# Kernel optimization log

Measured on AMD Instinct MI355X. Metric: run time of the kernel, lower is better.

The kernel has to match this reference:

```python
import jax, jax.numpy as jnp
import numpy as np

N_NODES = 100000
N_EDGES = 1600000
HIDDEN = 64


def setup_inputs() -> dict:
    key = jax.random.key(0)
    ks = jax.random.split(key, 12)
    x = jax.random.normal(ks[0], (N_NODES, HIDDEN), dtype=jnp.float32)
    edge_index = jax.random.randint(ks[1], (2, N_EDGES), 0, N_NODES, dtype=jnp.int64)
    s = 1.0 / np.sqrt(HIDDEN)  # glorot-ish scale for 64x64 linears
    params = {}
    for li, base in enumerate([2, 5, 8]):
        i = li + 1
        params[f"W_l{i}"] = jax.random.uniform(ks[base], (HIDDEN, HIDDEN), jnp.float32, -s, s)
        params[f"b_l{i}"] = jnp.zeros((HIDDEN,), jnp.float32)
        params[f"W_r{i}"] = jax.random.uniform(ks[base + 1], (HIDDEN, HIDDEN), jnp.float32, -s, s)
    return {"x": x, "edge_index": edge_index, **params}


def _sage_conv(x, src, dst, W_l, b_l, W_r):
    # mean-aggregate source features onto targets (PyG SAGEConv, aggr='mean')
    agg = jax.ops.segment_sum(x[src], dst, num_segments=N_NODES)  # [N, d]
    deg = jax.ops.segment_sum(jnp.ones_like(dst, dtype=x.dtype), dst, num_segments=N_NODES)
    agg = agg / jnp.maximum(deg, 1.0)[:, None]
    # out = lin_l(agg) + lin_r(x)
    return agg @ W_l + b_l + x @ W_r


def reference(x, edge_index, W_l1, b_l1, W_r1, W_l2, b_l2, W_r2, W_l3, b_l3, W_r3):
    src, dst = edge_index[0], edge_index[1]
    # eval mode: dropout is identity
    h = jax.nn.elu(_sage_conv(x, src, dst, W_l1, b_l1, W_r1))
    h = jax.nn.elu(_sage_conv(h, src, dst, W_l2, b_l2, W_r2))
    h = jax.nn.elu(_sage_conv(h, src, dst, W_l3, b_l3, W_r3))
    return h
```

## Files before the change

kernel.cpp:

```cpp
#include <hip/hip_runtime.h>
#include <hip/hip_bf16.h>
#include <math.h>


#define HID   64
#define SB    512
#define MAXSB 256
#define SCAP  10240
#define CHUNK 8192

__device__ __forceinline__ float b2f(unsigned short u) {
    unsigned int t = ((unsigned int)u) << 16;
    return __uint_as_float(t);
}
__device__ __forceinline__ unsigned short f2b(float f) {
    unsigned int u = __float_as_uint(f);
    u = (u + 0x7FFF + ((u >> 16) & 1)) >> 16;
    return (unsigned short)u;
}


__launch_bounds__(256)
__global__ void partition_edges(const int* __restrict__ src, const int* __restrict__ dst,
                                unsigned int* __restrict__ part, int* __restrict__ gcnt,
                                int E) {
    __shared__ unsigned int stage[CHUNK];
    __shared__ int lcnt[MAXSB];
    __shared__ int lbase[MAXSB];
    __shared__ int lrun[MAXSB];
    __shared__ int gpos[MAXSB];
    __shared__ int tmp[MAXSB];
    int tid = threadIdx.x;
    int e0 = blockIdx.x * CHUNK, e1 = min(e0 + CHUNK, E);

    lcnt[tid] = 0;
    __syncthreads();
    for (int e = e0 + tid; e < e1; e += 256)
        atomicAdd(&lcnt[dst[e] >> 9], 1);
    __syncthreads();
    int v = lcnt[tid];
    tmp[tid] = v;
    __syncthreads();
    for (int off = 1; off < 256; off <<= 1) {
        int u = (tid >= off) ? tmp[tid - off] : 0;
        __syncthreads();
        tmp[tid] += u;
        __syncthreads();
    }
    lbase[tid] = tmp[tid] - v;
    lrun[tid]  = tmp[tid] - v;
    __syncthreads();
    for (int e = e0 + tid; e < e1; e += 256) {
        int d = dst[e];
        int s = d >> 9;
        int pos = atomicAdd(&lrun[s], 1);
        stage[pos] = ((unsigned)(d & 511) << 17) | (unsigned)src[e];
    }
    __syncthreads();
    {
        int c = lcnt[tid];
        gpos[tid] = c ? atomicAdd(&gcnt[tid], c) : 0;
    }
    __syncthreads();
    for (int s = 0; s < MAXSB; ++s) {
        int c = lcnt[s];
        if (c == 0) continue;
        int gp = gpos[s];
        int c2 = min(c, max(SCAP - gp, 0));
        unsigned int* dp = part + (size_t)s * SCAP + gp;
        const unsigned int* sp = &stage[lbase[s]];
        for (int j = tid; j < c2; j += 256) dp[j] = sp[j];
    }
}


__launch_bounds__(256)
__global__ void sub_count(const unsigned int* __restrict__ part,
                          const int* __restrict__ gcnt, int* __restrict__ cnt, int N) {
    __shared__ int lcnt[SB];
    int s = blockIdx.x;
    int sz = min(gcnt[s], SCAP);
    const unsigned int* slab = part + (size_t)s * SCAP;
    for (int i = threadIdx.x; i < SB; i += 256) lcnt[i] = 0;
    __syncthreads();
    for (int i = threadIdx.x; i < sz; i += 256)
        atomicAdd(&lcnt[slab[i] >> 17], 1);
    __syncthreads();
    int base = s * SB;
    for (int i = threadIdx.x; i < SB; i += 256)
        if (base + i < N) cnt[base + i] = lcnt[i];
}


__launch_bounds__(256)
__global__ void sub_fill(const unsigned int* __restrict__ part,
                         const int* __restrict__ gcnt, const int* __restrict__ offs,
                         int* __restrict__ csr, int N) {
    __shared__ unsigned int stage[SCAP];
    __shared__ int lrun[SB];
    int s = blockIdx.x;
    int sz = min(gcnt[s], SCAP);
    const unsigned int* slab = part + (size_t)s * SCAP;
    int base = s * SB;
    int gbase = offs[base];
    for (int i = threadIdx.x; i < SB; i += 256) {
        int node = base + i;
        lrun[i] = offs[min(node, N)] - gbase;
    }
    __syncthreads();
    for (int i = threadIdx.x; i < sz; i += 256) {
        unsigned int u = slab[i];
        int pos = atomicAdd(&lrun[u >> 17], 1);
        stage[pos] = u & 0x1FFFF;
    }
    __syncthreads();
    int total = offs[min(base + SB, N)] - gbase;
    for (int j = threadIdx.x; j < total; j += 256)
        csr[gbase + j] = (int)stage[j];
}


__global__ void scan_partials(const int* __restrict__ cnt, int* __restrict__ bsum, int n) {
    __shared__ int lsum[256];
    int t = threadIdx.x;
    int base = blockIdx.x * 1024 + t * 4;
    int s = 0;
    if (base + 3 < n) {
        int4 v = *(const int4*)&cnt[base];
        s = v.x + v.y + v.z + v.w;
    } else {
        for (int i = 0; i < 4; ++i) if (base + i < n) s += cnt[base + i];
    }
    lsum[t] = s;
    __syncthreads();
    for (int off = 128; off > 0; off >>= 1) {
        if (t < off) lsum[t] += lsum[t + off];
        __syncthreads();
    }
    if (t == 0) bsum[blockIdx.x] = lsum[0];
}

__global__ void scan_tops(int* __restrict__ bsum, int* __restrict__ offs_last,
                          int nb, int E) {
    __shared__ int s[128];
    int t = threadIdx.x;
    s[t] = (t < nb) ? bsum[t] : 0;
    __syncthreads();
    for (int off = 1; off < 128; off <<= 1) {
        int v = (t >= off) ? s[t - off] : 0;
        __syncthreads();
        s[t] += v;
        __syncthreads();
    }
    if (t < nb) bsum[t] = (t == 0) ? 0 : s[t - 1];
    if (t == 0) *offs_last = E;
}

__global__ void scan_write(const int* __restrict__ cnt, const int* __restrict__ bsum,
                           int* __restrict__ offs, int n) {
    __shared__ int lsum[256];
    int t = threadIdx.x;
    int base = blockIdx.x * 1024 + t * 4;
    int v0 = 0, v1 = 0, v2 = 0, v3 = 0;
    bool full = (base + 3 < n);
    if (full) {
        int4 v = *(const int4*)&cnt[base];
        v0 = v.x; v1 = v.y; v2 = v.z; v3 = v.w;
    } else {
        if (base     < n) v0 = cnt[base];
        if (base + 1 < n) v1 = cnt[base + 1];
        if (base + 2 < n) v2 = cnt[base + 2];
        if (base + 3 < n) v3 = cnt[base + 3];
    }
    lsum[t] = v0 + v1 + v2 + v3;
    __syncthreads();
    for (int off = 1; off < 256; off <<= 1) {
        int u = (t >= off) ? lsum[t - off] : 0;
        __syncthreads();
        lsum[t] += u;
        __syncthreads();
    }
    int ex = bsum[blockIdx.x] + ((t == 0) ? 0 : lsum[t - 1]);
    int o0 = ex, o1 = ex + v0, o2 = o1 + v1, o3 = o2 + v2;
    if (full) {
        *(int4*)&offs[base] = make_int4(o0, o1, o2, o3);
    } else {
        if (base     < n) offs[base]     = o0;
        if (base + 1 < n) offs[base + 1] = o1;
        if (base + 2 < n) offs[base + 2] = o2;
        if (base + 3 < n) offs[base + 3] = o3;
    }
}


__global__ void to_bf16(const float* __restrict__ in, unsigned short* __restrict__ o, int n4) {
    int i = blockIdx.x * blockDim.x + threadIdx.x;
    if (i < n4) {
        float4 v = ((const float4*)in)[i];
        ushort4 u;
        u.x = f2b(v.x); u.y = f2b(v.y); u.z = f2b(v.z); u.w = f2b(v.w);
        ((ushort4*)o)[i] = u;
    }
}


__launch_bounds__(256)
__global__ void gather_mean(const unsigned short* __restrict__ hb,
                            const int* __restrict__ offs, const int* __restrict__ csr,
                            unsigned short* __restrict__ agg, int nnodes) {
    int lane = threadIdx.x & 63;
    int wv   = threadIdx.x >> 6;
    int wid  = blockIdx.x * 4 + wv;
    int nw   = gridDim.x * 4;
    for (int n = wid; n < nnodes; n += nw) {
        int beg = offs[n], end = offs[n + 1];
        int deg = end - beg;
        float a0 = 0.f, a1 = 0.f, a2 = 0.f, a3 = 0.f;
        float a4 = 0.f, a5 = 0.f, a6 = 0.f, a7 = 0.f;
        for (int base = beg; base < end; base += 64) {
            int cnt = min(64, end - base);
            int myi = csr[base + min(lane, cnt - 1)];
            int j = 0;
            for (; j + 8 <= cnt; j += 8) {
                int s0 = __shfl(myi, j + 0), s1 = __shfl(myi, j + 1);
                int s2 = __shfl(myi, j + 2), s3 = __shfl(myi, j + 3);
                int s4 = __shfl(myi, j + 4), s5 = __shfl(myi, j + 5);
                int s6 = __shfl(myi, j + 6), s7 = __shfl(myi, j + 7);
                a0 += b2f(hb[(size_t)s0 * HID + lane]);
                a1 += b2f(hb[(size_t)s1 * HID + lane]);
                a2 += b2f(hb[(size_t)s2 * HID + lane]);
                a3 += b2f(hb[(size_t)s3 * HID + lane]);
                a4 += b2f(hb[(size_t)s4 * HID + lane]);
                a5 += b2f(hb[(size_t)s5 * HID + lane]);
                a6 += b2f(hb[(size_t)s6 * HID + lane]);
                a7 += b2f(hb[(size_t)s7 * HID + lane]);
            }
            for (; j < cnt; ++j) {
                int s = __shfl(myi, j);
                a0 += b2f(hb[(size_t)s * HID + lane]);
            }
        }
        float m = (((a0 + a1) + (a2 + a3)) + ((a4 + a5) + (a6 + a7)))
                  * (1.0f / (float)max(deg, 1));
        agg[(size_t)n * HID + lane] = f2b(m);
    }
}


__launch_bounds__(256)
__global__ void dense_cat(const unsigned short* __restrict__ aggb,
                          const unsigned short* __restrict__ hb,
                          const float* __restrict__ Wl, const float* __restrict__ bl,
                          const float* __restrict__ Wr,
                          float* __restrict__ outf, unsigned short* __restrict__ out_bf,
                          int nrows) {
    __shared__ float W_s[128][64];
    __shared__ float cat_s[32][132];
    __shared__ float bl_s[64];
    int tid = threadIdx.x;
    int n0  = blockIdx.x * 32;

    for (int idx = tid; idx < 2048; idx += 256) {
        int f = idx >> 4, c4 = (idx & 15) * 4;
        const float* Wsrc = (f < 64) ? (Wl + f * 64 + c4) : (Wr + (f - 64) * 64 + c4);
        *(float4*)&W_s[f][c4] = *(const float4*)Wsrc;
    }
    if (tid < 64) bl_s[tid] = bl[tid];

    for (int idx = tid; idx < 1024; idx += 256) {
        int r = idx >> 5, c4 = idx & 31;
        float4 v = make_float4(0.f, 0.f, 0.f, 0.f);
        if (n0 + r < nrows) {
            const unsigned short* sp = (c4 < 16)
                ? (aggb + (size_t)(n0 + r) * HID + c4 * 4)
                : (hb   + (size_t)(n0 + r) * HID + (c4 - 16) * 4);
            ushort4 u = *(const ushort4*)sp;
            v = make_float4(b2f(u.x), b2f(u.y), b2f(u.z), b2f(u.w));
        }
        *(float4*)&cat_s[r][c4 * 4] = v;
    }
    __syncthreads();

    int cg = tid & 15, rg = tid >> 4;
    int c0 = cg * 4, r0 = rg * 2;
    float acc0x = 0.f, acc0y = 0.f, acc0z = 0.f, acc0w = 0.f;
    float acc1x = 0.f, acc1y = 0.f, acc1z = 0.f, acc1w = 0.f;

    for (int k = 0; k < 128; k += 4) {
        float4 a0 = *(float4*)&cat_s[r0 + 0][k];
        float4 a1 = *(float4*)&cat_s[r0 + 1][k];
#pragma unroll
        for (int u = 0; u < 4; ++u) {
            float4 w = *(float4*)&W_s[k + u][c0];
            float av0 = (&a0.x)[u], av1 = (&a1.x)[u];
            acc0x += av0 * w.x; acc0y += av0 * w.y;
            acc0z += av0 * w.z; acc0w += av0 * w.w;
            acc1x += av1 * w.x; acc1y += av1 * w.y;
            acc1z += av1 * w.z; acc1w += av1 * w.w;
        }
    }

    float bx = bl_s[c0], by = bl_s[c0 + 1], bz = bl_s[c0 + 2], bw = bl_s[c0 + 3];
#pragma unroll
    for (int i = 0; i < 2; ++i) {
        int row = n0 + r0 + i;
        if (row < nrows) {
            float4 o;
            o.x = (i ? acc1x : acc0x) + bx;
            o.y = (i ? acc1y : acc0y) + by;
            o.z = (i ? acc1z : acc0z) + bz;
            o.w = (i ? acc1w : acc0w) + bw;
            o.x = o.x > 0.f ? o.x : expm1f(o.x);
            o.y = o.y > 0.f ? o.y : expm1f(o.y);
            o.z = o.z > 0.f ? o.z : expm1f(o.z);
            o.w = o.w > 0.f ? o.w : expm1f(o.w);
            if (outf) *(float4*)&outf[(size_t)row * HID + c0] = o;
            if (out_bf) {
                ushort4 u;
                u.x = f2b(o.x); u.y = f2b(o.y); u.z = f2b(o.z); u.w = f2b(o.w);
                *(ushort4*)&out_bf[(size_t)row * HID + c0] = u;
            }
        }
    }
}


extern "C" void kernel_launch(void* const* d_in, const int* in_sizes, int n_in,
                              void* d_out, int out_size, void* d_ws, size_t ws_size,
                              hipStream_t stream) {
    const float* x   = (const float*)d_in[0];
    const int*   ei  = (const int*)d_in[1];
    const float* Wl1 = (const float*)d_in[2];
    const float* bl1 = (const float*)d_in[3];
    const float* Wr1 = (const float*)d_in[4];
    const float* Wl2 = (const float*)d_in[5];
    const float* bl2 = (const float*)d_in[6];
    const float* Wr2 = (const float*)d_in[7];
    const float* Wl3 = (const float*)d_in[8];
    const float* bl3 = (const float*)d_in[9];
    const float* Wr3 = (const float*)d_in[10];
    float* out = (float*)d_out;

    int N = in_sizes[0] / HID;
    int E = in_sizes[1] / 2;
    const int* src = ei;
    const int* dst = ei + E;

    int nsb = (N + SB - 1) / SB;
    int PB  = (E + CHUNK - 1) / CHUNK;
    int sb  = (N + 1023) / 1024;

    char* p = (char*)d_ws;
    unsigned short* aggB = (unsigned short*)p; p += (size_t)N * HID * 2;
    unsigned short* bfX  = (unsigned short*)p; p += (size_t)N * HID * 2;
    unsigned short* bf1  = (unsigned short*)p; p += (size_t)N * HID * 2;
    unsigned short* bf2  = (unsigned short*)p; p += (size_t)N * HID * 2;
    int*            csr  = (int*)p;            p += (size_t)E * sizeof(int);
    int*            cnt  = (int*)p;            p += (size_t)N * sizeof(int);
    int*            offs = (int*)p;            p += (size_t)(N + 4) * sizeof(int);
    int*            bsum = (int*)p;            p += 256 * sizeof(int);
    int*            gcnt = (int*)p;            p += MAXSB * sizeof(int);
    unsigned int*   part = (unsigned int*)p;   p += (size_t)MAXSB * SCAP * 4;

    hipMemsetAsync(gcnt, 0, MAXSB * sizeof(int), stream);

    partition_edges<<<PB, 256, 0, stream>>>(src, dst, part, gcnt, E);
    sub_count<<<nsb, 256, 0, stream>>>(part, gcnt, cnt, N);
    scan_partials<<<sb, 256, 0, stream>>>(cnt, bsum, N);
    scan_tops<<<1, 128, 0, stream>>>(bsum, &offs[N], sb, E);
    scan_write<<<sb, 256, 0, stream>>>(cnt, bsum, offs, N);
    sub_fill<<<nsb, 256, 0, stream>>>(part, gcnt, offs, csr, N);

    to_bf16<<<(N * HID / 4 + 255) / 256, 256, 0, stream>>>(x, bfX, N * HID / 4);

    int db = (N + 31) / 32;

    gather_mean<<<2048, 256, 0, stream>>>(bfX, offs, csr, aggB, N);
    dense_cat<<<db, 256, 0, stream>>>(aggB, bfX, Wl1, bl1, Wr1, (float*)nullptr, bf1, N);

    gather_mean<<<2048, 256, 0, stream>>>(bf1, offs, csr, aggB, N);
    dense_cat<<<db, 256, 0, stream>>>(aggB, bf1, Wl2, bl2, Wr2, (float*)nullptr, bf2, N);

    gather_mean<<<2048, 256, 0, stream>>>(bf2, offs, csr, aggB, N);
    dense_cat<<<db, 256, 0, stream>>>(aggB, bf2, Wl3, bl3, Wr3, out, (unsigned short*)nullptr, N);
}
```

Baseline: 445.0 us.

## Shrink partition chunks, use wave-shuffle scan, flatten per-bucket scatter loop

Cuts the edges per partition block from 8192 to 2048, so the grid has four times as many blocks. The shared-memory Hillis-Steele scan, which needed many block barriers, becomes a wavefront shuffle scan plus a small cross-wave offset. The serial loop over 256 buckets in the write-out becomes one flat loop over staged edges, using a per-edge bucket byte to find each global position. This removes barrier and serialization overhead, at the cost of more global atomics on the bucket counters and less contiguous write-out.

After: 404.0 us. 9.2% less time.

```diff
diff --git a/kernel.cpp b/kernel.cpp
--- a/kernel.cpp
+++ b/kernel.cpp
@@ -7,7 +7,7 @@
 #define SB    512
 #define MAXSB 256
 #define SCAP  10240
-#define CHUNK 8192
+#define CHUNK 2048
 
 __device__ __forceinline__ float b2f(unsigned short u) {
     unsigned int t = ((unsigned int)u) << 16;
@@ -25,36 +25,45 @@
                                 unsigned int* __restrict__ part, int* __restrict__ gcnt,
                                 int E) {
     __shared__ unsigned int stage[CHUNK];
+    __shared__ unsigned char sbkt[CHUNK];
     __shared__ int lcnt[MAXSB];
     __shared__ int lbase[MAXSB];
     __shared__ int lrun[MAXSB];
     __shared__ int gpos[MAXSB];
-    __shared__ int tmp[MAXSB];
-    int tid = threadIdx.x;
+    __shared__ int wtot[4];
+    int tid = threadIdx.x, w = tid >> 6, lane = tid & 63;
     int e0 = blockIdx.x * CHUNK, e1 = min(e0 + CHUNK, E);
+    int ne = e1 - e0;
+    if (ne <= 0) return;
 
     lcnt[tid] = 0;
     __syncthreads();
     for (int e = e0 + tid; e < e1; e += 256)
         atomicAdd(&lcnt[dst[e] >> 9], 1);
     __syncthreads();
-    int v = lcnt[tid];
-    tmp[tid] = v;
-    __syncthreads();
-    for (int off = 1; off < 256; off <<= 1) {
-        int u = (tid >= off) ? tmp[tid - off] : 0;
-        __syncthreads();
-        tmp[tid] += u;
-        __syncthreads();
-    }
-    lbase[tid] = tmp[tid] - v;
-    lrun[tid]  = tmp[tid] - v;
+    {
+        int orig = lcnt[tid];
+        int v = orig;
+#pragma unroll
+        for (int off = 1; off < 64; off <<= 1) {
+            int u = __shfl_up(v, off);
+            if (lane >= off) v += u;
+        }
+        if (lane == 63) wtot[w] = v;
+        __syncthreads();
+        int woff = 0;
+        for (int i = 0; i < w; ++i) woff += wtot[i];
+        int excl = v + woff - orig;
+        lbase[tid] = excl;
+        lrun[tid]  = excl;
+    }
     __syncthreads();
     for (int e = e0 + tid; e < e1; e += 256) {
         int d = dst[e];
         int s = d >> 9;
         int pos = atomicAdd(&lrun[s], 1);
         stage[pos] = ((unsigned)(d & 511) << 17) | (unsigned)src[e];
+        sbkt[pos]  = (unsigned char)s;
     }
     __syncthreads();
     {
@@ -62,14 +71,10 @@
         gpos[tid] = c ? atomicAdd(&gcnt[tid], c) : 0;
     }
     __syncthreads();
-    for (int s = 0; s < MAXSB; ++s) {
-        int c = lcnt[s];
-        if (c == 0) continue;
-        int gp = gpos[s];
-        int c2 = min(c, max(SCAP - gp, 0));
-        unsigned int* dp = part + (size_t)s * SCAP + gp;
-        const unsigned int* sp = &stage[lbase[s]];
-        for (int j = tid; j < c2; j += 256) dp[j] = sp[j];
+    for (int j = tid; j < ne; j += 256) {
+        int s = sbkt[j];
+        int gp = gpos[s] + (j - lbase[s]);
+        if (gp < SCAP) part[(size_t)s * SCAP + gp] = stage[j];
     }
 }
 
```
